# Kernel tuning notes

Hardware: AMD Instinct MI355X
Metric: run time of the kernel (lower is better)

## Reference

```python
import jax, jax.numpy as jnp
import numpy as np

E = 512   # embed_dim
H = 8     # num_heads
DH = E // H  # head_dim = 64
L = 1024  # tgt_len (language tokens)
S = 1024  # src_len (video/audio tokens)
B = 8     # batch
EPS = 1e-8


def setup_inputs() -> dict:
    key = jax.random.key(0)
    ks = jax.random.split(key, 12)
    xavier = float(np.sqrt(2.0 / (E + E)))
    inp = {
        "query": jax.random.normal(ks[0], (L, B, E), jnp.float32),
        "mod1": jax.random.normal(ks[1], (S, B, E), jnp.float32),
        "mod2": jax.random.normal(ks[2], (S, B, E), jnp.float32),
    }
    wnames = ["Wq", "Wk1", "Wk2", "Wv1", "Wv2", "Wg1", "Wg2", "Wo"]
    for i, n in enumerate(wnames):
        inp[n] = jax.random.normal(ks[3 + i], (E, E), jnp.float32) * xavier
        inp["b" + n[1:]] = jnp.zeros((E,), jnp.float32)
    return inp


def _heads(x):
    # (T, B, E) -> (B*H, T, DH), fairseq-style head split
    T = x.shape[0]
    return x.reshape(T, B * H, DH).transpose(1, 0, 2)


def reference(query, mod1, mod2,
              Wq, bq, Wk1, bk1, Wk2, bk2,
              Wv1, bv1, Wv2, bv2,
              Wg1, bg1, Wg2, bg2, Wo, bo):
    scaling = DH ** -0.5
    q = (query @ Wq.T + bq) * scaling          # (L, B, E)
    k1 = mod1 @ Wk1.T + bk1                    # (S, B, E)
    k2 = mod2 @ Wk2.T + bk2
    # gated values: v_i * sigmoid(gate_i(mod_i)), summed across modalities
    v = ((mod1 @ Wv1.T + bv1) * jax.nn.sigmoid(mod1 @ Wg1.T + bg1)
         + (mod2 @ Wv2.T + bv2) * jax.nn.sigmoid(mod2 @ Wg2.T + bg2))

    qh, k1h, k2h, vh = _heads(q), _heads(k1), _heads(k2), _heads(v)  # (B*H, T, DH)

    # 3x3 Gram determinant scores (computed via GEMMs, no [B,L,S,D] broadcast)
    ll = jnp.sum(qh * qh, -1)[:, :, None]        # (BH, L, 1)
    vv = jnp.sum(k1h * k1h, -1)[:, None, :]      # (BH, 1, S)
    aa = jnp.sum(k2h * k2h, -1)[:, None, :]
    va = jnp.sum(k1h * k2h, -1)[:, None, :]
    lv = jnp.einsum('bld,bsd->bls', qh, k1h)     # (BH, L, S)
    la = jnp.einsum('bld,bsd->bls', qh, k2h)
    det = (ll * (vv * aa - va * va)
           - lv * (lv * aa - la * va)
           + la * (lv * va - la * vv))
    scores = -jnp.sqrt(jnp.clip(det, EPS))       # (BH, L, S)

    attn = jax.nn.softmax(scores, axis=-1)
    out = jnp.einsum('bls,bsd->bld', attn, vh)   # (BH, L, DH)
    out = out.transpose(1, 0, 2).reshape(L, B, E)
    return out @ Wo.T + bo                       # (L, B, E)
```

## Files before the change

### kernel.cpp

```cpp
#include <hip/hip_runtime.h>
#include <math.h>


typedef short bf16x8 __attribute__((ext_vector_type(8)));
typedef float f32x4  __attribute__((ext_vector_type(4)));

#define MFMA16(a,b,c) __builtin_amdgcn_mfma_f32_16x16x32_bf16((a),(b),(c),0,0,0)

static constexpr float LOG2E_F = 1.4426950408889634f;
static constexpr float CBRT_L2E = 1.12994722f;
static constexpr float DEFER_THR = 11.54156033f;
static constexpr float EPS_SCALED = 2.0813689e-8f;

typedef const __attribute__((address_space(1))) unsigned int gas_u32;
typedef __attribute__((address_space(3))) unsigned int las_u32;

__device__ __forceinline__ void gload16(const void* g, void* l){
  __builtin_amdgcn_global_load_lds((gas_u32*)g, (las_u32*)l, 16, 0, 0);
}

__device__ __forceinline__ float b2f(unsigned short s){
  union { unsigned u; float f; } v; v.u = ((unsigned)s) << 16; return v.f;
}
__device__ __forceinline__ unsigned short f2b(float f){
  union { float f; unsigned u; } v; v.f = f;
  unsigned r = v.u + 0x7fffu + ((v.u >> 16) & 1u);
  return (unsigned short)(r >> 16);
}

__global__ __launch_bounds__(256) void split3_kernel(
    const float* __restrict__ a, const float* __restrict__ b,
    const float* __restrict__ c,
    unsigned short* __restrict__ hi, unsigned short* __restrict__ lo, int n)
{
  const int y = blockIdx.y;
  const float* src = (y == 0) ? a : ((y == 1) ? b : c);
  unsigned short* h = hi + (size_t)y * n;
  unsigned short* L = lo + (size_t)y * n;
  int stride = gridDim.x * 256;
  for (int i = blockIdx.x*256 + threadIdx.x; i < n; i += stride){
    float v = src[i];
    unsigned short hh = f2b(v);
    h[i] = hh;
    L[i] = f2b(v - b2f(hh));
  }
}

__global__ __launch_bounds__(256) void splitW_kernel(
    const float* w0, const float* w1, const float* w2, const float* w3,
    const float* w4, const float* w5, const float* w6, const float* w7,
    unsigned short* __restrict__ hi, unsigned short* __restrict__ lo, int n)
{
  const int y = blockIdx.y;
  const float* src = w0;
  if (y == 1) src = w1; if (y == 2) src = w2; if (y == 3) src = w3;
  if (y == 4) src = w4; if (y == 5) src = w5; if (y == 6) src = w6;
  if (y == 7) src = w7;
  unsigned short* h = hi + (size_t)y * n;
  unsigned short* L = lo + (size_t)y * n;
  int stride = gridDim.x * 256;
  for (int i = blockIdx.x*256 + threadIdx.x; i < n; i += stride){
    float v = src[i];
    unsigned short hh = f2b(v);
    h[i] = hh;
    L[i] = f2b(v - b2f(hh));
  }
}

enum { EPI_F32 = 0, EPI_HEADS = 1, EPI_GATE = 2 };

template<int NPASS, int EPI, bool ACCUM>
__global__ __launch_bounds__(256,1) void gemm128_kernel(
    const unsigned short* __restrict__ Ahi, const unsigned short* __restrict__ Alo,
    const unsigned short* __restrict__ Bhi, const unsigned short* __restrict__ Blo,
    const unsigned short* __restrict__ Bg,
    const float* __restrict__ bias, const float* __restrict__ biasg,
    float scale,
    float* __restrict__ outF,
    unsigned short* __restrict__ outHi, unsigned short* __restrict__ outLo)
{
  constexpr int iAhi = 0;
  constexpr int iAlo = 1;
  constexpr int iBhi = (NPASS == 3) ? 2 : 1;
  constexpr int iBlo = iBhi + 1;
  constexpr int iBg  = iBlo + 1;
  constexpr int NARR = (EPI == EPI_GATE) ? 5 : ((NPASS == 3) ? 4 : 3);
  __shared__ unsigned short smem[2*NARR*4096];

  const int tid = threadIdx.x, w = tid >> 6, l = tid & 63;
  const int r0 = blockIdx.x * 128, e0 = blockIdx.y * 128;
  const int lrow = l & 15, kg = l >> 4;

  f32x4 acc[4][4];
  #pragma unroll
  for (int m = 0; m < 4; ++m)
    #pragma unroll
    for (int n = 0; n < 4; ++n) acc[m][n] = (f32x4){0.f,0.f,0.f,0.f};
  f32x4 gacc[4][4];
  if constexpr (EPI == EPI_GATE){
    #pragma unroll
    for (int m = 0; m < 4; ++m)
      #pragma unroll
      for (int n = 0; n < 4; ++n) gacc[m][n] = (f32x4){0.f,0.f,0.f,0.f};
  }

  const int sgsw = ((l & 3) ^ ((l >> 3) & 3)) * 8;
  const int srA = r0 + w*16 + (l >> 2);
  const int srB = e0 + w*16 + (l >> 2);

  auto stage = [&](int buf, int kk){
    const int lb = buf*NARR*4096 + w*512;
    #pragma unroll
    for (int j = 0; j < 2; ++j){
      const size_t ga = (size_t)(srA + j*64)*512 + kk + sgsw;
      const size_t gb = (size_t)(srB + j*64)*512 + kk + sgsw;
      gload16(&Ahi[ga], &smem[lb + iAhi*4096 + j*2048]);
      if constexpr (NPASS == 3)
        gload16(&Alo[ga], &smem[lb + iAlo*4096 + j*2048]);
      gload16(&Bhi[gb], &smem[lb + iBhi*4096 + j*2048]);
      gload16(&Blo[gb], &smem[lb + iBlo*4096 + j*2048]);
      if constexpr (EPI == EPI_GATE)
        gload16(&Bg[gb], &smem[lb + iBg*4096 + j*2048]);
    }
  };

  const int rowA = (w >> 1)*64 + lrow;
  const int rowB = (w & 1)*64 + lrow;
  const int kgs  = (kg ^ ((lrow >> 1) & 3)) * 8;

  auto compute = [&](int buf){
    const int bb = buf*NARR*4096;
    bf16x8 ah[4], al[4];
    #pragma unroll
    for (int m = 0; m < 4; ++m){
      const int ra = (rowA + m*16)*32 + kgs;
      ah[m] = *(const bf16x8*)&smem[bb + iAhi*4096 + ra];
      if constexpr (NPASS == 3)
        al[m] = *(const bf16x8*)&smem[bb + iAlo*4096 + ra];
    }
    #pragma unroll
    for (int n = 0; n < 4; ++n){
      const int rb = (rowB + n*16)*32 + kgs;
      bf16x8 bh = *(const bf16x8*)&smem[bb + iBhi*4096 + rb];
      bf16x8 bl = *(const bf16x8*)&smem[bb + iBlo*4096 + rb];
      #pragma unroll
      for (int m = 0; m < 4; ++m){
        acc[m][n] = MFMA16(ah[m], bh, acc[m][n]);
        acc[m][n] = MFMA16(ah[m], bl, acc[m][n]);
        if constexpr (NPASS == 3)
          acc[m][n] = MFMA16(al[m], bh, acc[m][n]);
      }
      if constexpr (EPI == EPI_GATE){
        bf16x8 bg = *(const bf16x8*)&smem[bb + iBg*4096 + rb];
        #pragma unroll
        for (int m = 0; m < 4; ++m)
          gacc[m][n] = MFMA16(ah[m], bg, gacc[m][n]);
      }
    }
  };

  stage(0, 0);
  __syncthreads();
  for (int t = 0; t < 16; ++t){
    if (t < 15) stage((t+1) & 1, (t+1)*32);
    compute(t & 1);
    __syncthreads();
  }

  #pragma unroll
  for (int n = 0; n < 4; ++n){
    const int e = e0 + (w & 1)*64 + n*16 + lrow;
    const float bv = bias[e];
    float bgv;
    if constexpr (EPI == EPI_GATE) bgv = biasg[e];
    #pragma unroll
    for (int m = 0; m < 4; ++m){
      #pragma unroll
      for (int q = 0; q < 4; ++q){
        const int r = r0 + (w >> 1)*64 + m*16 + kg*4 + q;
        if constexpr (EPI == EPI_F32){
          outF[(size_t)r*512 + e] = (acc[m][n][q] + bv) * scale;
        } else if constexpr (EPI == EPI_HEADS){
          const float y = (acc[m][n][q] + bv) * scale;
          const int bh = ((r & 7) << 3) + (e >> 6);
          const size_t off = ((size_t)bh*1024 + (r >> 3))*64 + (e & 63);
          unsigned short hh = f2b(y);
          outHi[off] = hh;
          outLo[off] = f2b(y - b2f(hh));
        } else {
          const float yv = acc[m][n][q] + bv;
          const float yg = gacc[m][n][q] + bgv;
          const float sg = 1.0f / (1.0f + exp2f(-yg * LOG2E_F));
          float o = yv * sg;
          if constexpr (ACCUM) o += outF[(size_t)r*512 + e];
          outF[(size_t)r*512 + e] = o;
        }
      }
    }
  }
}

__global__ __launch_bounds__(256) void norms_kernel(
    const unsigned short* __restrict__ qh, const unsigned short* __restrict__ ql,
    const unsigned short* __restrict__ k1h, const unsigned short* __restrict__ k1l,
    const unsigned short* __restrict__ k2h, const unsigned short* __restrict__ k2l,
    float* __restrict__ ll, f32x4* __restrict__ nrm4)
{
  const int idx = blockIdx.x*256 + threadIdx.x;
  const size_t base = (size_t)idx * 64;
  float sll = 0.f, svv = 0.f, saa = 0.f, sva = 0.f;
  #pragma unroll
  for (int j = 0; j < 8; ++j){
    bf16x8 q_h = *(const bf16x8*)&qh[base + j*8];
    bf16x8 q_l = *(const bf16x8*)&ql[base + j*8];
    bf16x8 a_h = *(const bf16x8*)&k1h[base + j*8];
    bf16x8 a_l = *(const bf16x8*)&k1l[base + j*8];
    bf16x8 c_h = *(const bf16x8*)&k2h[base + j*8];
    bf16x8 c_l = *(const bf16x8*)&k2l[base + j*8];
    #pragma unroll
    for (int i = 0; i < 8; ++i){
      float qv = b2f((unsigned short)q_h[i]) + b2f((unsigned short)q_l[i]);
      float a1 = b2f((unsigned short)a_h[i]) + b2f((unsigned short)a_l[i]);
      float a2 = b2f((unsigned short)c_h[i]) + b2f((unsigned short)c_l[i]);
      sll += qv*qv; svv += a1*a1; saa += a2*a2; sva += a1*a2;
    }
  }
  ll[idx] = sll;
  nrm4[idx] = (f32x4){svv*saa - sva*sva, saa, 2.0f*sva, svv};
}

__global__ __launch_bounds__(256) void vtrans_kernel(
    const float* __restrict__ v, unsigned short* __restrict__ vTh)
{
  __shared__ unsigned short sH[64*64];
  const int bh = blockIdx.y, b = bh >> 3, h = bh & 7;
  const int s0 = blockIdx.x * 64;
  const int tid = threadIdx.x;
  for (int c = tid; c < 1024; c += 256){
    const int i = c >> 4, sl = c & 15;
    const size_t g = ((size_t)(s0 + i)*8 + b)*512 + h*64 + sl*4;
    f32x4 a = *(const f32x4*)&v[g];
    #pragma unroll
    for (int e = 0; e < 4; ++e)
      sH[(sl*4 + e)*64 + i] = f2b(a[e]);
  }
  __syncthreads();
  for (int c = tid; c < 512; c += 256){
    const int d = c >> 3, sl = c & 7;
    const size_t g = ((size_t)bh*64 + d)*1024 + s0 + sl*8;
    *(bf16x8*)&vTh[g] = *(const bf16x8*)&sH[d*64 + sl*8];
  }
}

__global__ __launch_bounds__(256,2) void attn_kernel(
    const unsigned short* __restrict__ qhh, const unsigned short* __restrict__ qhl,
    const unsigned short* __restrict__ k1hh, const unsigned short* __restrict__ k1hl,
    const unsigned short* __restrict__ k2hh, const unsigned short* __restrict__ k2hl,
    const unsigned short* __restrict__ vTh,
    const float* __restrict__ llv, const f32x4* __restrict__ nrm4,
    unsigned short* __restrict__ aoHi)
{
  __shared__ unsigned short sK1h[4096];
  __shared__ unsigned short sK1l[4096];
  __shared__ unsigned short sK2h[4096];
  __shared__ unsigned short sK2l[4096];
  __shared__ unsigned short sVh[4096];
  __shared__ unsigned short sPh[8192];
  __shared__ f32x4 sN4[64];

  const int bh = blockIdx.y, l0 = blockIdx.x * 128;
  const int tid = threadIdx.x, w = tid >> 6, lane = tid & 63;
  const int lrow = lane & 15, kg = lane >> 4;

  bf16x8 qfh[2][2], qfl[2][2];
  #pragma unroll
  for (int m = 0; m < 2; ++m){
    const size_t qb = ((size_t)bh*1024 + l0 + w*32 + m*16 + lrow)*64 + kg*8;
    qfh[m][0] = *(const bf16x8*)&qhh[qb];
    qfl[m][0] = *(const bf16x8*)&qhl[qb];
    qfh[m][1] = *(const bf16x8*)&qhh[qb + 32];
    qfl[m][1] = *(const bf16x8*)&qhl[qb + 32];
  }
  float ll_r[2][4];
  #pragma unroll
  for (int m = 0; m < 2; ++m)
    #pragma unroll
    for (int q = 0; q < 4; ++q)
      ll_r[m][q] = llv[bh*1024 + l0 + w*32 + m*16 + kg*4 + q];

  f32x4 accO[2][4];
  #pragma unroll
  for (int m = 0; m < 2; ++m)
    #pragma unroll
    for (int i = 0; i < 4; ++i) accO[m][i] = (f32x4){0.f,0.f,0.f,0.f};
  float mn[2][4], s_run[2][4];
  #pragma unroll
  for (int m = 0; m < 2; ++m)
    #pragma unroll
    for (int q = 0; q < 4; ++q){ mn[m][q] = 1e30f; s_run[m][q] = 0.f; }

  const int c0 = tid, c1 = tid + 256;
  const int r0g = c0 >> 3, g0 = ((c0 & 7) ^ (r0g & 7)) * 8;
  const int r1g = c1 >> 3, g1 = ((c1 & 7) ^ (r1g & 7)) * 8;

  for (int ss = 0; ss < 1024; ss += 64){
    {
      const size_t kb = (size_t)bh*1024 + ss;
      const size_t k0 = (kb + r0g)*64 + g0;
      const size_t k1_ = (kb + r1g)*64 + g1;
      gload16(&k1hh[k0], &sK1h[c0*8]);  gload16(&k1hh[k1_], &sK1h[c1*8]);
      gload16(&k1hl[k0], &sK1l[c0*8]);  gload16(&k1hl[k1_], &sK1l[c1*8]);
      gload16(&k2hh[k0], &sK2h[c0*8]);  gload16(&k2hh[k1_], &sK2h[c1*8]);
      gload16(&k2hl[k0], &sK2l[c0*8]);  gload16(&k2hl[k1_], &sK2l[c1*8]);
      const size_t v0 = ((size_t)bh*64 + r0g)*1024 + ss + g0;
      const size_t v1 = ((size_t)bh*64 + r1g)*1024 + ss + g1;
      gload16(&vTh[v0], &sVh[c0*8]);    gload16(&vTh[v1], &sVh[c1*8]);
      if (tid < 64) gload16(&nrm4[(size_t)bh*1024 + ss + tid], &sN4[tid]);
    }
    __syncthreads();

    float p_[2][4][4];
    float tmn[2][4];
    #pragma unroll
    for (int m = 0; m < 2; ++m)
      #pragma unroll
      for (int q = 0; q < 4; ++q) tmn[m][q] = 1e30f;

    #pragma unroll
    for (int nt = 0; nt < 4; ++nt){
      f32x4 lv[2], la[2];
      #pragma unroll
      for (int m = 0; m < 2; ++m){ lv[m] = (f32x4){0.f,0.f,0.f,0.f}; la[m] = (f32x4){0.f,0.f,0.f,0.f}; }
      #pragma unroll
      for (int ks = 0; ks < 2; ++ks){
        const int row = nt*16 + lrow;
        const int off = row*64 + (((ks*4 + kg) ^ (row & 7)) * 8);
        bf16x8 b1h = *(const bf16x8*)&sK1h[off];
        bf16x8 b1l = *(const bf16x8*)&sK1l[off];
        bf16x8 b2h = *(const bf16x8*)&sK2h[off];
        bf16x8 b2l = *(const bf16x8*)&sK2l[off];
        #pragma unroll
        for (int m = 0; m < 2; ++m){
          lv[m] = MFMA16(qfh[m][ks], b1h, lv[m]);
          lv[m] = MFMA16(qfh[m][ks], b1l, lv[m]);
          lv[m] = MFMA16(qfl[m][ks], b1h, lv[m]);
          la[m] = MFMA16(qfh[m][ks], b2h, la[m]);
          la[m] = MFMA16(qfh[m][ks], b2l, la[m]);
          la[m] = MFMA16(qfl[m][ks], b2h, la[m]);
        }
      }
      f32x4 n4 = sN4[nt*16 + lrow];
      const float cross = n4[0], c_aa = n4[1], c_va2 = n4[2], c_vv = n4[3];
      #pragma unroll
      for (int m = 0; m < 2; ++m){
        #pragma unroll
        for (int q = 0; q < 4; ++q){
          const float flv = lv[m][q], fla = la[m][q];
          float t = fmaf(-c_vv, fla*fla, (flv*fla)*c_va2);
          t = fmaf(-c_aa, flv*flv, t);
          const float det = fmaf(ll_r[m][q], cross, t);
          const float sq = __builtin_amdgcn_sqrtf(fmaxf(det, EPS_SCALED));
          p_[m][nt][q] = sq;
          tmn[m][q] = fminf(tmn[m][q], sq);
        }
      }
    }
    #pragma unroll
    for (int m = 0; m < 2; ++m)
      #pragma unroll
      for (int q = 0; q < 4; ++q){
        tmn[m][q] = fminf(tmn[m][q], __shfl_xor(tmn[m][q], 1));
        tmn[m][q] = fminf(tmn[m][q], __shfl_xor(tmn[m][q], 2));
        tmn[m][q] = fminf(tmn[m][q], __shfl_xor(tmn[m][q], 4));
        tmn[m][q] = fminf(tmn[m][q], __shfl_xor(tmn[m][q], 8));
      }
    int up = 0;
    #pragma unroll
    for (int m = 0; m < 2; ++m)
      #pragma unroll
      for (int q = 0; q < 4; ++q) up |= (tmn[m][q] < mn[m][q] - DEFER_THR) ? 1 : 0;
    if (__any(up)){
      #pragma unroll
      for (int m = 0; m < 2; ++m)
        #pragma unroll
        for (int q = 0; q < 4; ++q){
          const float mnn = fminf(mn[m][q], tmn[m][q]);
          const float rs = __builtin_amdgcn_exp2f(mnn - mn[m][q]);
          mn[m][q] = mnn;
          s_run[m][q] *= rs;
          #pragma unroll
          for (int dt = 0; dt < 4; ++dt) accO[m][dt][q] *= rs;
        }
    }
    float ps[2][4];
    #pragma unroll
    for (int m = 0; m < 2; ++m)
      #pragma unroll
      for (int q = 0; q < 4; ++q) ps[m][q] = 0.f;
    #pragma unroll
    for (int nt = 0; nt < 4; ++nt)
      #pragma unroll
      for (int m = 0; m < 2; ++m)
        #pragma unroll
        for (int q = 0; q < 4; ++q){
          const float e = __builtin_amdgcn_exp2f(mn[m][q] - p_[m][nt][q]);
          p_[m][nt][q] = e;
          ps[m][q] += e;
        }
    #pragma unroll
    for (int m = 0; m < 2; ++m)
      #pragma unroll
      for (int q = 0; q < 4; ++q){
        float v = ps[m][q];
        v += __shfl_xor(v, 1); v += __shfl_xor(v, 2);
        v += __shfl_xor(v, 4); v += __shfl_xor(v, 8);
        s_run[m][q] += v;
      }

    #pragma unroll
    for (int m = 0; m < 2; ++m){
      #pragma unroll
      for (int nt = 0; nt < 4; ++nt){
        const int col = nt*16 + lrow;
        const int cg = col >> 3, cr = col & 7;
        #pragma unroll
        for (int qp = 0; qp < 2; ++qp){
          unsigned int pk;
          asm("v_cvt_pk_bf16_f32 %0, %1, %2" : "=v"(pk)
              : "v"(p_[m][nt][qp*2]), "v"(p_[m][nt][qp*2+1]));
          const int ra = m*16 + kg*4 + qp*2, rb = ra + 1;
          sPh[w*2048 + ra*64 + ((cg ^ (ra & 7))*8) + cr] = (unsigned short)(pk & 0xffffu);
          sPh[w*2048 + rb*64 + ((cg ^ (rb & 7))*8) + cr] = (unsigned short)(pk >> 16);
        }
      }
    }

    #pragma unroll
    for (int ks = 0; ks < 2; ++ks){
      bf16x8 pa[2];
      #pragma unroll
      for (int m = 0; m < 2; ++m){
        const int prow = m*16 + lrow;
        pa[m] = *(const bf16x8*)&sPh[w*2048 + prow*64 + (((ks*4 + kg) ^ (prow & 7))*8)];
      }
      #pragma unroll
      for (int dt = 0; dt < 4; ++dt){
        const int vrow = dt*16 + lrow;
        bf16x8 bvh = *(const bf16x8*)&sVh[vrow*64 + (((ks*4 + kg) ^ (vrow & 7))*8)];
        #pragma unroll
        for (int m = 0; m < 2; ++m)
          accO[m][dt] = MFMA16(pa[m], bvh, accO[m][dt]);
      }
    }
    __syncthreads();
  }

  const int b = bh >> 3, h = bh & 7;
  #pragma unroll
  for (int m = 0; m < 2; ++m){
    float rcp[4];
    #pragma unroll
    for (int q = 0; q < 4; ++q) rcp[q] = __builtin_amdgcn_rcpf(s_run[m][q]);
    #pragma unroll
    for (int dt = 0; dt < 4; ++dt){
      const int d = dt*16 + lrow;
      #pragma unroll
      for (int q = 0; q < 4; ++q){
        const int l_ = l0 + w*32 + m*16 + kg*4 + q;
        aoHi[((size_t)l_*8 + b)*512 + h*64 + d] = f2b(accO[m][dt][q] * rcp[q]);
      }
    }
  }
}

extern "C" void kernel_launch(void* const* d_in, const int* in_sizes, int n_in,
                              void* d_out, int out_size, void* d_ws, size_t ws_size,
                              hipStream_t stream)
{
  const float* query = (const float*)d_in[0];
  const float* mod1  = (const float*)d_in[1];
  const float* mod2  = (const float*)d_in[2];
  const float* bq  = (const float*)d_in[4];
  const float* bk1 = (const float*)d_in[6];
  const float* bk2 = (const float*)d_in[8];
  const float* bv1 = (const float*)d_in[10];
  const float* bv2 = (const float*)d_in[12];
  const float* bg1 = (const float*)d_in[14];
  const float* bg2 = (const float*)d_in[16];
  const float* bo  = (const float*)d_in[18];

  char* p = (char*)d_ws;
  auto take = [&](size_t bytes) -> char* {
    char* r = p; p += (bytes + 255) & ~(size_t)255; return r;
  };
  const size_t NX = (size_t)8192*512;
  const size_t NW = (size_t)512*512;
  const size_t XB = NX*2, WB = NW*2;
  const size_t HB = (size_t)64*1024*64*2;
  const size_t FB = NX*4;
  const size_t NB = (size_t)64*1024*4;

  unsigned short* xhi = (unsigned short*)take(3*XB);
  unsigned short* xlo = (unsigned short*)take(3*XB);
  unsigned short* whi = (unsigned short*)take(8*WB);
  unsigned short* wlo = (unsigned short*)take(8*WB);
  unsigned short* qh_hi  = (unsigned short*)take(HB);
  unsigned short* qh_lo  = (unsigned short*)take(HB);
  unsigned short* k1h_hi = (unsigned short*)take(HB);
  unsigned short* k1h_lo = (unsigned short*)take(HB);
  unsigned short* k2h_hi = (unsigned short*)take(HB);
  unsigned short* k2h_lo = (unsigned short*)take(HB);
  unsigned short* vT_hi  = (unsigned short*)take(HB);
  float* vacc = (float*)take(FB);
  unsigned short* ao_hi = (unsigned short*)take(HB);
  float* llv = (float*)take(NB);
  f32x4* nrm4 = (f32x4*)take(4*NB);

  unsigned short* xq_hi = xhi;            unsigned short* xq_lo = xlo;
  unsigned short* x1_hi = xhi + NX;       unsigned short* x1_lo = xlo + NX;
  unsigned short* x2_hi = xhi + 2*NX;     unsigned short* x2_lo = xlo + 2*NX;

  split3_kernel<<<dim3(1024,3), 256, 0, stream>>>(query, mod1, mod2, xhi, xlo, (int)NX);
  splitW_kernel<<<dim3(256,8), 256, 0, stream>>>(
      (const float*)d_in[3], (const float*)d_in[5], (const float*)d_in[7],
      (const float*)d_in[9], (const float*)d_in[11], (const float*)d_in[13],
      (const float*)d_in[15], (const float*)d_in[17], whi, wlo, (int)NW);

  dim3 gg(64, 4);
  gemm128_kernel<3,EPI_HEADS,false><<<gg, 256, 0, stream>>>(
      xq_hi, xq_lo, whi + 0*NW, wlo + 0*NW, nullptr, bq, nullptr,
      0.125f*CBRT_L2E, nullptr, qh_hi, qh_lo);
  gemm128_kernel<3,EPI_HEADS,false><<<gg, 256, 0, stream>>>(
      x1_hi, x1_lo, whi + 1*NW, wlo + 1*NW, nullptr, bk1, nullptr,
      CBRT_L2E, nullptr, k1h_hi, k1h_lo);
  gemm128_kernel<3,EPI_HEADS,false><<<gg, 256, 0, stream>>>(
      x2_hi, x2_lo, whi + 2*NW, wlo + 2*NW, nullptr, bk2, nullptr,
      CBRT_L2E, nullptr, k2h_hi, k2h_lo);
  gemm128_kernel<3,EPI_GATE,false><<<gg, 256, 0, stream>>>(
      x1_hi, x1_lo, whi + 3*NW, wlo + 3*NW, whi + 5*NW, bv1, bg1, 1.0f,
      vacc, nullptr, nullptr);
  gemm128_kernel<3,EPI_GATE,true><<<gg, 256, 0, stream>>>(
      x2_hi, x2_lo, whi + 4*NW, wlo + 4*NW, whi + 6*NW, bv2, bg2, 1.0f,
      vacc, nullptr, nullptr);

  norms_kernel<<<256, 256, 0, stream>>>(qh_hi, qh_lo, k1h_hi, k1h_lo,
                                        k2h_hi, k2h_lo, llv, nrm4);
  vtrans_kernel<<<dim3(16, 64), 256, 0, stream>>>(vacc, vT_hi);

  attn_kernel<<<dim3(8, 64), 256, 0, stream>>>(
      qh_hi, qh_lo, k1h_hi, k1h_lo, k2h_hi, k2h_lo, vT_hi,
      llv, nrm4, ao_hi);

  gemm128_kernel<2,EPI_F32,false><<<gg, 256, 0, stream>>>(
      ao_hi, nullptr, whi + 7*NW, wlo + 7*NW, nullptr, bo, nullptr, 1.0f,
      (float*)d_out, nullptr, nullptr);
}
```

Baseline: 418.4 us.

## Merge five projection GEMMs into one launch and retile the output GEMM

Replaces the five separate projection GEMM launches with a single proj_kernel over a 64x20 grid, where each block picks its job (q, k1, k2, gated v1, gated v2). The two gated value results now go to separate buffers and are summed in the transpose kernel, which removes the read-modify-write accumulation and the ordering dependency between them. The output GEMM moves to a 64-row tile with 512 blocks, and the attention grid is flattened so consecutive blocks cover different heads. The goal is more blocks in flight with less tail imbalance and fewer launches, at the cost of runtime branching inside the fused kernel, extra register pressure from gacc in every job, and an extra fp32 buffer.

```diff
diff --git a/kernel.cpp b/kernel.cpp
--- a/kernel.cpp
+++ b/kernel.cpp
@@ -67,60 +67,59 @@
   }
 }
 
-enum { EPI_F32 = 0, EPI_HEADS = 1, EPI_GATE = 2 };
-
-template<int NPASS, int EPI, bool ACCUM>
-__global__ __launch_bounds__(256,1) void gemm128_kernel(
-    const unsigned short* __restrict__ Ahi, const unsigned short* __restrict__ Alo,
-    const unsigned short* __restrict__ Bhi, const unsigned short* __restrict__ Blo,
-    const unsigned short* __restrict__ Bg,
-    const float* __restrict__ bias, const float* __restrict__ biasg,
-    float scale,
-    float* __restrict__ outF,
-    unsigned short* __restrict__ outHi, unsigned short* __restrict__ outLo)
-{
-  constexpr int iAhi = 0;
-  constexpr int iAlo = 1;
-  constexpr int iBhi = (NPASS == 3) ? 2 : 1;
-  constexpr int iBlo = iBhi + 1;
-  constexpr int iBg  = iBlo + 1;
-  constexpr int NARR = (EPI == EPI_GATE) ? 5 : ((NPASS == 3) ? 4 : 3);
-  __shared__ unsigned short smem[2*NARR*4096];
-
+__global__ __launch_bounds__(256,2) void proj_kernel(
+    const unsigned short* __restrict__ xhi, const unsigned short* __restrict__ xlo,
+    const unsigned short* __restrict__ whi, const unsigned short* __restrict__ wlo,
+    const float* __restrict__ bq, const float* __restrict__ bk1,
+    const float* __restrict__ bk2,
+    const float* __restrict__ bv1, const float* __restrict__ bg1,
+    const float* __restrict__ bv2, const float* __restrict__ bg2,
+    unsigned short* __restrict__ qh_hi, unsigned short* __restrict__ qh_lo,
+    unsigned short* __restrict__ k1h_hi, unsigned short* __restrict__ k1h_lo,
+    unsigned short* __restrict__ k2h_hi, unsigned short* __restrict__ k2h_lo,
+    float* __restrict__ vacc1, float* __restrict__ vacc2)
+{
+  __shared__ unsigned short smem[2*4*4096];
   const int tid = threadIdx.x, w = tid >> 6, l = tid & 63;
-  const int r0 = blockIdx.x * 128, e0 = blockIdx.y * 128;
+  const int y = blockIdx.y;
+  const int job = y >> 2;
+  const int r0 = blockIdx.x * 128, e0 = (y & 3) * 128;
   const int lrow = l & 15, kg = l >> 4;
-
-  f32x4 acc[4][4];
+  const bool isGate = (job >= 3);
+
+  const size_t NXs = (size_t)8192*512, NWs = (size_t)512*512;
+  const int aidx = (job == 0) ? 0 : ((job == 1 || job == 3) ? 1 : 2);
+  const unsigned short* Ahi = xhi + (size_t)aidx * NXs;
+  const unsigned short* Alo = xlo + (size_t)aidx * NXs;
+  const int bidx = isGate ? ((job == 3) ? 3 : 4) : job;
+  const unsigned short* Bhi = whi + (size_t)bidx * NWs;
+  const unsigned short* Blo = wlo + (size_t)bidx * NWs;
+  const unsigned short* Bg  = whi + (size_t)((job == 3) ? 5 : 6) * NWs;
+
+  f32x4 acc[4][4], gacc[4][4];
   #pragma unroll
   for (int m = 0; m < 4; ++m)
     #pragma unroll
-    for (int n = 0; n < 4; ++n) acc[m][n] = (f32x4){0.f,0.f,0.f,0.f};
-  f32x4 gacc[4][4];
-  if constexpr (EPI == EPI_GATE){
-    #pragma unroll
-    for (int m = 0; m < 4; ++m)
-      #pragma unroll
-      for (int n = 0; n < 4; ++n) gacc[m][n] = (f32x4){0.f,0.f,0.f,0.f};
-  }
+    for (int n = 0; n < 4; ++n){
+      acc[m][n] = (f32x4){0.f,0.f,0.f,0.f};
+      gacc[m][n] = (f32x4){0.f,0.f,0.f,0.f};
+    }
 
   const int sgsw = ((l & 3) ^ ((l >> 3) & 3)) * 8;
   const int srA = r0 + w*16 + (l >> 2);
   const int srB = e0 + w*16 + (l >> 2);
 
   auto stage = [&](int buf, int kk){
-    const int lb = buf*NARR*4096 + w*512;
+    const int lb = buf*4*4096 + w*512;
     #pragma unroll
     for (int j = 0; j < 2; ++j){
       const size_t ga = (size_t)(srA + j*64)*512 + kk + sgsw;
       const size_t gb = (size_t)(srB + j*64)*512 + kk + sgsw;
-      gload16(&Ahi[ga], &smem[lb + iAhi*4096 + j*2048]);
-      if constexpr (NPASS == 3)
-        gload16(&Alo[ga], &smem[lb + iAlo*4096 + j*2048]);
-      gload16(&Bhi[gb], &smem[lb + iBhi*4096 + j*2048]);
-      gload16(&Blo[gb], &smem[lb + iBlo*4096 + j*2048]);
-      if constexpr (EPI == EPI_GATE)
-        gload16(&Bg[gb], &smem[lb + iBg*4096 + j*2048]);
+      gload16(&Ahi[ga], &smem[lb + 0*4096 + j*2048]);
+      if (!isGate) gload16(&Alo[ga], &smem[lb + 1*4096 + j*2048]);
+      else         gload16(&Bg[gb],  &smem[lb + 1*4096 + j*2048]);
+      gload16(&Bhi[gb], &smem[lb + 2*4096 + j*2048]);
+      gload16(&Blo[gb], &smem[lb + 3*4096 + j*2048]);
     }
   };
 
@@ -129,29 +128,30 @@
   const int kgs  = (kg ^ ((lrow >> 1) & 3)) * 8;
 
   auto compute = [&](int buf){
-    const int bb = buf*NARR*4096;
+    const int bb = buf*4*4096;
     bf16x8 ah[4], al[4];
     #pragma unroll
     for (int m = 0; m < 4; ++m){
       const int ra = (rowA + m*16)*32 + kgs;
-      ah[m] = *(const bf16x8*)&smem[bb + iAhi*4096 + ra];
-      if constexpr (NPASS == 3)
-        al[m] = *(const bf16x8*)&smem[bb + iAlo*4096 + ra];
+      ah[m] = *(const bf16x8*)&smem[bb + ra];
+      if (!isGate) al[m] = *(const bf16x8*)&smem[bb + 4096 + ra];
     }
     #pragma unroll
     for (int n = 0; n < 4; ++n){
       const int rb = (rowB + n*16)*32 + kgs;
-      bf16x8 bh = *(const bf16x8*)&smem[bb + iBhi*4096 + rb];
-      bf16x8 bl = *(const bf16x8*)&smem[bb + iBlo*4096 + rb];
+      bf16x8 bh = *(const bf16x8*)&smem[bb + 8192 + rb];
+      bf16x8 bl = *(const bf16x8*)&smem[bb + 12288 + rb];
       #pragma unroll
       for (int m = 0; m < 4; ++m){
         acc[m][n] = MFMA16(ah[m], bh, acc[m][n]);
         acc[m][n] = MFMA16(ah[m], bl, acc[m][n]);
-        if constexpr (NPASS == 3)
+      }
+      if (!isGate){
+        #pragma unroll
+        for (int m = 0; m < 4; ++m)
           acc[m][n] = MFMA16(al[m], bh, acc[m][n]);
-      }
-      if constexpr (EPI == EPI_GATE){
-        bf16x8 bg = *(const bf16x8*)&smem[bb + iBg*4096 + rb];
+      } else {
+        bf16x8 bg = *(const bf16x8*)&smem[bb + 4096 + rb];
         #pragma unroll
         for (int m = 0; m < 4; ++m)
           gacc[m][n] = MFMA16(ah[m], bg, gacc[m][n]);
@@ -167,34 +167,124 @@
     __syncthreads();
   }
 
+  if (!isGate){
+    const float* bias = (job == 0) ? bq : ((job == 1) ? bk1 : bk2);
+    const float scale = (job == 0) ? 0.125f*CBRT_L2E : CBRT_L2E;
+    unsigned short* oH = (job == 0) ? qh_hi : ((job == 1) ? k1h_hi : k2h_hi);
+    unsigned short* oL = (job == 0) ? qh_lo : ((job == 1) ? k1h_lo : k2h_lo);
+    #pragma unroll
+    for (int n = 0; n < 4; ++n){
+      const int e = e0 + (w & 1)*64 + n*16 + lrow;
+      const float bv = bias[e];
+      #pragma unroll
+      for (int m = 0; m < 4; ++m){
+        #pragma unroll
+        for (int q = 0; q < 4; ++q){
+          const int r = r0 + (w >> 1)*64 + m*16 + kg*4 + q;
+          const float yv = (acc[m][n][q] + bv) * scale;
+          const int bh = ((r & 7) << 3) + (e >> 6);
+          const size_t off = ((size_t)bh*1024 + (r >> 3))*64 + (e & 63);
+          unsigned short hh = f2b(yv);
+          oH[off] = hh;
+          oL[off] = f2b(yv - b2f(hh));
+        }
+      }
+    }
+  } else {
+    const float* bvv = (job == 3) ? bv1 : bv2;
+    const float* bgg = (job == 3) ? bg1 : bg2;
+    float* outF = (job == 3) ? vacc1 : vacc2;
+    #pragma unroll
+    for (int n = 0; n < 4; ++n){
+      const int e = e0 + (w & 1)*64 + n*16 + lrow;
+      const float bv = bvv[e], bg_ = bgg[e];
+      #pragma unroll
+      for (int m = 0; m < 4; ++m){
+        #pragma unroll
+        for (int q = 0; q < 4; ++q){
+          const int r = r0 + (w >> 1)*64 + m*16 + kg*4 + q;
+          const float yv = acc[m][n][q] + bv;
+          const float yg = gacc[m][n][q] + bg_;
+          const float sg = 1.0f / (1.0f + exp2f(-yg * LOG2E_F));
+          outF[(size_t)r*512 + e] = yv * sg;
+        }
+      }
+    }
+  }
+}
+
+__global__ __launch_bounds__(256,2) void gemmout_kernel(
+    const unsigned short* __restrict__ Ahi,
+    const unsigned short* __restrict__ Bhi, const unsigned short* __restrict__ Blo,
+    const float* __restrict__ bias, float* __restrict__ outF)
+{
+  __shared__ unsigned short smem[2*10240];
+  const int tid = threadIdx.x, w = tid >> 6, l = tid & 63;
+  const int r0 = blockIdx.x * 64, e0 = blockIdx.y * 128;
+  const int lrow = l & 15, kg = l >> 4;
+
+  f32x4 acc[2][4];
+  #pragma unroll
+  for (int m = 0; m < 2; ++m)
+    #pragma unroll
+    for (int n = 0; n < 4; ++n) acc[m][n] = (f32x4){0.f,0.f,0.f,0.f};
+
+  const int sgsw = ((l & 3) ^ ((l >> 3) & 3)) * 8;
+  const int srA = r0 + w*16 + (l >> 2);
+  const int srB = e0 + w*16 + (l >> 2);
+
+  auto stage = [&](int buf, int kk){
+    const int lb = buf*10240;
+    gload16(&Ahi[(size_t)srA*512 + kk + sgsw], &smem[lb + tid*8]);
+    #pragma unroll
+    for (int j = 0; j < 2; ++j){
+      const size_t gb = (size_t)(srB + j*64)*512 + kk + sgsw;
+      gload16(&Bhi[gb], &smem[lb + 2048 + (tid + j*256)*8]);
+      gload16(&Blo[gb], &smem[lb + 6144 + (tid + j*256)*8]);
+    }
+  };
+
+  const int rowA = (w >> 1)*32 + lrow;
+  const int rowB = (w & 1)*64 + lrow;
+  const int kgs  = (kg ^ ((lrow >> 1) & 3)) * 8;
+
+  auto compute = [&](int buf){
+    const int bb = buf*10240;
+    bf16x8 ah[2];
+    #pragma unroll
+    for (int m = 0; m < 2; ++m)
+      ah[m] = *(const bf16x8*)&smem[bb + (rowA + m*16)*32 + kgs];
+    #pragma unroll
+    for (int n = 0; n < 4; ++n){
+      const int rb = (rowB + n*16)*32 + kgs;
+      bf16x8 bh = *(const bf16x8*)&smem[bb + 2048 + rb];
+      bf16x8 bl = *(const bf16x8*)&smem[bb + 6144 + rb];
+      #pragma unroll
+      for (int m = 0; m < 2; ++m){
+        acc[m][n] = MFMA16(ah[m], bh, acc[m][n]);
+        acc[m][n] = MFMA16(ah[m], bl, acc[m][n]);
+      }
+    }
+  };
+
+  stage(0, 0);
+  __syncthreads();
+  for (int t = 0; t < 16; ++t){
+    if (t < 15) stage((t+1) & 1, (t+1)*32);
+    compute(t & 1);
+    __syncthreads();
+  }
+
   #pragma unroll
   for (int n = 0; n < 4; ++n){
     const int e = e0 + (w & 1)*64 + n*16 + lrow;
     const float bv = bias[e];
-    float bgv;
-    if constexpr (EPI == EPI_GATE) bgv = biasg[e];
-    #pragma unroll
-    for (int m = 0; m < 4; ++m){
+    #pragma unroll
+    for (int m = 0; m < 2; ++m){
       #pragma unroll
       for (int q = 0; q < 4; ++q){
-        const int r = r0 + (w >> 1)*64 + m*16 + kg*4 + q;
-        if constexpr (EPI == EPI_F32){
-          outF[(size_t)r*512 + e] = (acc[m][n][q] + bv) * scale;
-        } else if constexpr (EPI == EPI_HEADS){
-          const float y = (acc[m][n][q] + bv) * scale;
-          const int bh = ((r & 7) << 3) + (e >> 6);
-          const size_t off = ((size_t)bh*1024 + (r >> 3))*64 + (e & 63);
-          unsigned short hh = f2b(y);
-          outHi[off] = hh;
-          outLo[off] = f2b(y - b2f(hh));
-        } else {
-          const float yv = acc[m][n][q] + bv;
-          const float yg = gacc[m][n][q] + bgv;
-          const float sg = 1.0f / (1.0f + exp2f(-yg * LOG2E_F));
-          float o = yv * sg;
-          if constexpr (ACCUM) o += outF[(size_t)r*512 + e];
-          outF[(size_t)r*512 + e] = o;
-        }
+        const int r = r0 + (w >> 1)*32 + m*16 + kg*4 + q;
+        outF[(size_t)r*512 + e] = acc[m][n][q] + bv;
       }
     }
   }
@@ -230,7 +320,8 @@
 }
 
 __global__ __launch_bounds__(256) void vtrans_kernel(
-    const float* __restrict__ v, unsigned short* __restrict__ vTh)
+    const float* __restrict__ v1, const float* __restrict__ v2,
+    unsigned short* __restrict__ vTh)
 {
   __shared__ unsigned short sH[64*64];
   const int bh = blockIdx.y, b = bh >> 3, h = bh & 7;
@@ -239,10 +330,11 @@
   for (int c = tid; c < 1024; c += 256){
     const int i = c >> 4, sl = c & 15;
     const size_t g = ((size_t)(s0 + i)*8 + b)*512 + h*64 + sl*4;
-    f32x4 a = *(const f32x4*)&v[g];
+    f32x4 a = *(const f32x4*)&v1[g];
+    f32x4 bb = *(const f32x4*)&v2[g];
     #pragma unroll
     for (int e = 0; e < 4; ++e)
-      sH[(sl*4 + e)*64 + i] = f2b(a[e]);
+      sH[(sl*4 + e)*64 + i] = f2b(a[e] + bb[e]);
   }
   __syncthreads();
   for (int c = tid; c < 512; c += 256){
@@ -268,7 +360,7 @@
   __shared__ unsigned short sPh[8192];
   __shared__ f32x4 sN4[64];
 
-  const int bh = blockIdx.y, l0 = blockIdx.x * 128;
+  const int bh = blockIdx.x & 63, l0 = (blockIdx.x >> 6) * 128;
   const int tid = threadIdx.x, w = tid >> 6, lane = tid & 63;
   const int lrow = lane & 15, kg = lane >> 4;
 
@@ -511,14 +603,11 @@
   unsigned short* k2h_hi = (unsigned short*)take(HB);
   unsigned short* k2h_lo = (unsigned short*)take(HB);
   unsigned short* vT_hi  = (unsigned short*)take(HB);
-  float* vacc = (float*)take(FB);
+  float* vacc1 = (float*)take(FB);
+  float* vacc2 = (float*)take(FB);
   unsigned short* ao_hi = (unsigned short*)take(HB);
   float* llv = (float*)take(NB);
   f32x4* nrm4 = (f32x4*)take(4*NB);
-
-  unsigned short* xq_hi = xhi;            unsigned short* xq_lo = xlo;
-  unsigned short* x1_hi = xhi + NX;       unsigned short* x1_lo = xlo + NX;
-  unsigned short* x2_hi = xhi + 2*NX;     unsigned short* x2_lo = xlo + 2*NX;
 
   split3_kernel<<<dim3(1024,3), 256, 0, stream>>>(query, mod1, mod2, xhi, xlo, (int)NX);
   splitW_kernel<<<dim3(256,8), 256, 0, stream>>>(
@@ -526,32 +615,18 @@
       (const float*)d_in[9], (const float*)d_in[11], (const float*)d_in[13],
       (const float*)d_in[15], (const float*)d_in[17], whi, wlo, (int)NW);
 
-  dim3 gg(64, 4);
-  gemm128_kernel<3,EPI_HEADS,false><<<gg, 256, 0, stream>>>(
-      xq_hi, xq_lo, whi + 0*NW, wlo + 0*NW, nullptr, bq, nullptr,
-      0.125f*CBRT_L2E, nullptr, qh_hi, qh_lo);
-  gemm128_kernel<3,EPI_HEADS,false><<<gg, 256, 0, stream>>>(
-      x1_hi, x1_lo, whi + 1*NW, wlo + 1*NW, nullptr, bk1, nullptr,
-      CBRT_L2E, nullptr, k1h_hi, k1h_lo);
-  gemm128_kernel<3,EPI_HEADS,false><<<gg, 256, 0, stream>>>(
-      x2_hi, x2_lo, whi + 2*NW, wlo + 2*NW, nullptr, bk2, nullptr,
-      CBRT_L2E, nullptr, k2h_hi, k2h_lo);
-  gemm128_kernel<3,EPI_GATE,false><<<gg, 256, 0, stream>>>(
-      x1_hi, x1_lo, whi + 3*NW, wlo + 3*NW, whi + 5*NW, bv1, bg1, 1.0f,
-      vacc, nullptr, nullptr);
-  gemm128_kernel<3,EPI_GATE,true><<<gg, 256, 0, stream>>>(
-      x2_hi, x2_lo, whi + 4*NW, wlo + 4*NW, whi + 6*NW, bv2, bg2, 1.0f,
-      vacc, nullptr, nullptr);
+  proj_kernel<<<dim3(64, 20), 256, 0, stream>>>(
+      xhi, xlo, whi, wlo, bq, bk1, bk2, bv1, bg1, bv2, bg2,
+      qh_hi, qh_lo, k1h_hi, k1h_lo, k2h_hi, k2h_lo, vacc1, vacc2);
 
   norms_kernel<<<256, 256, 0, stream>>>(qh_hi, qh_lo, k1h_hi, k1h_lo,
                                         k2h_hi, k2h_lo, llv, nrm4);
-  vtrans_kernel<<<dim3(16, 64), 256, 0, stream>>>(vacc, vT_hi);
-
-  attn_kernel<<<dim3(8, 64), 256, 0, stream>>>(
+  vtrans_kernel<<<dim3(16, 64), 256, 0, stream>>>(vacc1, vacc2, vT_hi);
+
+  attn_kernel<<<512, 256, 0, stream>>>(
       qh_hi, qh_lo, k1h_hi, k1h_lo, k2h_hi, k2h_lo, vT_hi,
       llv, nrm4, ao_hi);
 
-  gemm128_kernel<2,EPI_F32,false><<<gg, 256, 0, stream>>>(
-      ao_hi, nullptr, whi + 7*NW, wlo + 7*NW, nullptr, bo, nullptr, 1.0f,
-      (float*)d_out, nullptr, nullptr);
-}
+  gemmout_kernel<<<dim3(128, 4), 256, 0, stream>>>(
+      ao_hi, whi + 7*NW, wlo + 7*NW, bo, (float*)d_out);
+}
```

New measurement: 371.0 us. -11.3%, faster.
